# Optimization experiments

Measured on AMD Instinct MI355X. Metric: run time of the kernel, lower is better.

The kernel has to match this reference:

```python
import jax, jax.numpy as jnp
import numpy as np

H = 8        # num attention heads
DH = 160     # head dim (hidden_size // H)
HS = 1280    # hidden_size
CAD = 768    # cross_attention_dim
R = 4        # LoRA rank
LORA_SCALE = 1.0  # `scale` forward arg (default 1.0)


def setup_inputs() -> dict:
    key = jax.random.key(0)
    ks = jax.random.split(key, 16)
    rn = lambda k, s, std=0.02: (jax.random.normal(k, s) * std).astype(jnp.float32)
    return {
        "hidden_states": jax.random.normal(ks[0], (8, 4096, HS), jnp.float32),
        "encoder_hidden_states": jax.random.normal(ks[1], (8, 77, CAD), jnp.float32),
        # base attention projections (nn.Linear weight layout: [out, in])
        "Wq": rn(ks[2], (HS, HS)),
        "Wk": rn(ks[3], (HS, CAD)),
        "Wv": rn(ks[4], (HS, CAD)),
        "Wo": rn(ks[5], (HS, HS)),
        "bo": jnp.zeros((HS,), jnp.float32),
        # LoRA down/up pairs (down std ~ 1/rank; up nonzero so grads flow)
        "q_down": rn(ks[6], (R, HS), 0.25), "q_up": rn(ks[7], (HS, R)),
        "k_down": rn(ks[8], (R, CAD), 0.25), "k_up": rn(ks[9], (HS, R)),
        "v_down": rn(ks[10], (R, CAD), 0.25), "v_up": rn(ks[11], (HS, R)),
        "o_down": rn(ks[12], (R, HS), 0.25), "o_up": rn(ks[13], (HS, R)),
    }


def reference(hidden_states, encoder_hidden_states, Wq, Wk, Wv, Wo, bo,
              q_down, q_up, k_down, k_up, v_down, v_up, o_down, o_up):
    B, S, _ = hidden_states.shape
    T = encoder_hidden_states.shape[1]
    lora = lambda x, d, u: (x @ d.T) @ u.T  # LoRALinearLayer: up(down(x))

    q = hidden_states @ Wq.T + LORA_SCALE * lora(hidden_states, q_down, q_up)
    k = encoder_hidden_states @ Wk.T + LORA_SCALE * lora(encoder_hidden_states, k_down, k_up)
    v = encoder_hidden_states @ Wv.T + LORA_SCALE * lora(encoder_hidden_states, v_down, v_up)

    q = q.reshape(B, S, H, DH)
    k = k.reshape(B, T, H, DH)
    v = v.reshape(B, T, H, DH)

    # attn.get_attention_scores: scaled QK^T, softmax (no mask)
    inv_sqrt_d = jnp.asarray(1.0 / np.sqrt(DH), q.dtype)
    scores = jnp.einsum('bshd,bthd->bhst', q, k) * inv_sqrt_d
    probs = jax.nn.softmax(scores, axis=-1)
    o = jnp.einsum('bhst,bthd->bshd', probs, v).reshape(B, S, H * DH)

    # to_out[0] (Linear with bias) + LoRA on the same input; to_out[1] dropout = identity (eval)
    return o @ Wo.T + bo + LORA_SCALE * lora(o, o_down, o_up)
```

## Files before the change

kernel.cpp:

```cpp
#include <hip/hip_runtime.h>
#include <hip/hip_bf16.h>
#include <stdint.h>

typedef short bf16x8 __attribute__((ext_vector_type(8)));
typedef float f32x4 __attribute__((ext_vector_type(4)));

#define DEVI static __device__ __forceinline__

DEVI ushort f2bf(float f) {
  union { float f; uint32_t u; } v; v.f = f;
  uint32_t u = v.u;
  return (ushort)((u + 0x7fffu + ((u >> 16) & 1u)) >> 16);
}

DEVI void gload16(const void* g, void* l) {
  __builtin_amdgcn_global_load_lds((const __attribute__((address_space(1))) void*)g,
                                   (__attribute__((address_space(3))) void*)l,
                                   16, 0, 0);
}

#define SB() __builtin_amdgcn_sched_barrier(0)
#define BAR() __builtin_amdgcn_s_barrier()
#define MFMA(a, b, c) __builtin_amdgcn_mfma_f32_16x16x32_bf16((a), (b), (c), 0, 0, 0)

DEVI int pair_src_row(int c, int* k8) {
  int pair = c >> 3;
  int s = (c & 7) ^ (pair & 7);
  *k8 = s >> 1;
  return pair * 2 + (s & 1);
}
DEVI int pair_frag_off(int r, int k8) {
  int p = (k8 * 2 + (r & 1)) ^ ((r >> 1) & 7);
  return (r >> 1) * 64 + p * 8;
}

__global__ __launch_bounds__(256) void prep(
    const float* __restrict__ hs, ushort* __restrict__ hs_bf,
    const float* __restrict__ Wq, const float* __restrict__ q_up, const float* __restrict__ q_down,
    ushort* __restrict__ WqT, float scale,
    const float* __restrict__ ehs, ushort* __restrict__ ehs_bf,
    const float* __restrict__ Wk, const float* __restrict__ k_up, const float* __restrict__ k_down,
    const float* __restrict__ Wv, const float* __restrict__ v_up, const float* __restrict__ v_down,
    ushort* __restrict__ Wkv,
    const float* __restrict__ Wo, const float* __restrict__ o_up, const float* __restrict__ o_down,
    ushort* __restrict__ Wo_bf, ushort* __restrict__ Nt)
{
  __shared__ ushort tile[64][66];
  const int b = blockIdx.x;
  const int tid = threadIdx.x;
  if (b < 2048) {
    const long step = 2048L * 256;
    for (long idx = (long)b * 256 + tid; idx < 5242880; idx += step) {
      const float4* p = (const float4*)(hs + idx * 8);
      float4 a = p[0], c = p[1];
      union { ushort us[8]; uint4 v; } r;
      r.us[0] = f2bf(a.x); r.us[1] = f2bf(a.y); r.us[2] = f2bf(a.z); r.us[3] = f2bf(a.w);
      r.us[4] = f2bf(c.x); r.us[5] = f2bf(c.y); r.us[6] = f2bf(c.z); r.us[7] = f2bf(c.w);
      *(uint4*)(hs_bf + idx * 8) = r.v;
    }
  } else if (b < 2448) {
    const int fb = b - 2048;
    const int o0 = (fb / 20) * 64, i0 = (fb % 20) * 64;
    const int lo = tid >> 6;
    const int li = tid & 63;
#pragma unroll
    for (int r = 0; r < 16; ++r) {
      int o = o0 + r * 4 + lo;
      int i = i0 + li;
      float v = Wq[(long)o * 1280 + i];
#pragma unroll
      for (int q = 0; q < 4; ++q) v += q_up[o * 4 + q] * q_down[q * 1280 + i];
      tile[li][r * 4 + lo] = f2bf(v * scale);
    }
    __syncthreads();
#pragma unroll
    for (int r = 0; r < 16; ++r) {
      int i = i0 + r * 4 + lo;
      WqT[(long)i * 1280 + o0 + li] = tile[r * 4 + lo][li];
    }
  } else {
    const int sb = b - 2448;
    if (sb < 231) {
      int idx = sb * 256 + tid;
      if (idx < 59136) {
        const float4* p = (const float4*)(ehs + (long)idx * 8);
        float4 a = p[0], c = p[1];
        union { ushort us[8]; uint4 v; } r;
        r.us[0] = f2bf(a.x); r.us[1] = f2bf(a.y); r.us[2] = f2bf(a.z); r.us[3] = f2bf(a.w);
        r.us[4] = f2bf(c.x); r.us[5] = f2bf(c.y); r.us[6] = f2bf(c.z); r.us[7] = f2bf(c.w);
        *(uint4*)(ehs_bf + (long)idx * 8) = r.v;
      }
    } else if (sb < 4071) {
      int idx = (sb - 231) * 256 + tid;
      int o = idx / 768, i = idx - o * 768;
      float v = Wk[idx];
#pragma unroll
      for (int q = 0; q < 4; ++q) v += k_up[o * 4 + q] * k_down[q * 768 + i];
      Wkv[idx] = f2bf(v);
    } else if (sb < 7911) {
      int idx = (sb - 4071) * 256 + tid;
      int o = idx / 768, i = idx - o * 768;
      float v = Wv[idx];
#pragma unroll
      for (int q = 0; q < 4; ++q) v += v_up[o * 4 + q] * v_down[q * 768 + i];
      Wkv[983040 + idx] = f2bf(v);
    } else if (sb < 14311) {
      int idx = (sb - 7911) * 256 + tid;
      int o = idx / 1280, i = idx - o * 1280;
      float v = Wo[idx];
#pragma unroll
      for (int q = 0; q < 4; ++q) v += o_up[o * 4 + q] * o_down[q * 1280 + i];
      Wo_bf[idx] = f2bf(v);
    } else {
      int idx = (sb - 14311) * 256 + tid;
      int bb = idx / (1280 * 24);
      int rem = idx % (1280 * 24);
      int j = rem / 24, q = rem % 24;
      int h = q / 3, t = 77 + q % 3;
      Nt[(long)bb * 1280 * 640 + (long)j * 640 + h * 80 + t] = 0;
    }
  }
}


DEVI void gemm_bt_body(int bx, int by, int z,
    const ushort* __restrict__ A, long sA0, long sA1, int lda, int validM,
    const ushort* __restrict__ B, long sB0, long sB1, int ldb, int validN,
    float* __restrict__ C32, ushort* __restrict__ C16, long sC0, long sC1, int ldc,
    const float* __restrict__ bias, int K, ushort* As, ushort* Bs)
{
  const ushort* Ab = A + (long)(z >> 3) * sA0 + (long)(z & 7) * sA1;
  const ushort* Bb = B + (long)(z >> 3) * sB0 + (long)(z & 7) * sB1;
  const int m0 = bx * 128;
  const int n0 = by * 128;
  const int tid = threadIdx.x;
  const int lane = tid & 63;
  const int wid = tid >> 6;

  const int c0 = tid;
  const int arow0 = min(m0 + (c0 >> 2), validM - 1);
  const int arow1 = min(m0 + (c0 >> 2) + 64, validM - 1);
  const int brow0 = min(n0 + (c0 >> 2), validN - 1);
  const int brow1 = min(n0 + (c0 >> 2) + 64, validN - 1);
  const int seg = (c0 & 3) * 8;

  const int wr = (wid >> 1) * 64;
  const int wc = (wid & 1) * 64;
  const int frow = lane & 15;
  const int fk = (lane >> 4) * 8;

  f32x4 acc[4][4] = {};

  for (int kt = 0; kt < K; kt += 32) {
    gload16(Ab + (long)arow0 * lda + kt + seg, As + c0 * 8);
    gload16(Ab + (long)arow1 * lda + kt + seg, As + (c0 + 256) * 8);
    gload16(Bb + (long)brow0 * ldb + kt + seg, Bs + c0 * 8);
    gload16(Bb + (long)brow1 * ldb + kt + seg, Bs + (c0 + 256) * 8);
    __syncthreads();

    bf16x8 af[4], bfr[4];
#pragma unroll
    for (int m = 0; m < 4; ++m)
      af[m] = *(const bf16x8*)(As + (wr + m * 16 + frow) * 32 + fk);
#pragma unroll
    for (int n = 0; n < 4; ++n)
      bfr[n] = *(const bf16x8*)(Bs + (wc + n * 16 + frow) * 32 + fk);
#pragma unroll
    for (int m = 0; m < 4; ++m)
#pragma unroll
      for (int n = 0; n < 4; ++n)
        acc[m][n] = MFMA(af[m], bfr[n], acc[m][n]);
    __syncthreads();
  }

  const long cb = (long)(z >> 3) * sC0 + (long)(z & 7) * sC1;
  const int crow = m0 + wr + (lane >> 4) * 4;
  const int ccol = n0 + wc + (lane & 15);
#pragma unroll
  for (int m = 0; m < 4; ++m)
#pragma unroll
    for (int n = 0; n < 4; ++n)
#pragma unroll
      for (int j = 0; j < 4; ++j) {
        int r = crow + m * 16 + j;
        int c = ccol + n * 16;
        if (r < validM && c < validN) {
          float v = acc[m][n][j];
          if (bias) v += bias[c];
          if (C32) C32[cb + (long)r * ldc + c] = v;
          else     C16[cb + (long)r * ldc + c] = f2bf(v);
        }
      }
}

__global__ __launch_bounds__(256) void gemm_bt(
    const ushort* A, long sA0, long sA1, int lda, int validM,
    const ushort* B, long sB0, long sB1, int ldb, int validN,
    float* C32, ushort* C16, long sC0, long sC1, int ldc,
    const float* bias, int K)
{
  __shared__ ushort As[128 * 32];
  __shared__ ushort Bs[128 * 32];
  gemm_bt_body(blockIdx.x, blockIdx.y, blockIdx.z,
               A, sA0, sA1, lda, validM, B, sB0, sB1, ldb, validN,
               C32, C16, sC0, sC1, ldc, bias, K, As, Bs);
}

__global__ __launch_bounds__(256) void gemm_mtnt(
    const ushort* __restrict__ kv_bf, const ushort* __restrict__ WqT,
    const ushort* __restrict__ Wo_bf, ushort* __restrict__ Mt, ushort* __restrict__ Nt)
{
  __shared__ ushort As[128 * 32];
  __shared__ ushort Bs[128 * 32];
  const int x = blockIdx.x, z = blockIdx.z;
  if (x < 10) {
    gemm_bt_body(x, 0, z, Wo_bf, 0, 160, 1280, 1280,
                 kv_bf + 1280, 77L * 2560, 160, 2560, 77,
                 nullptr, Nt, 1280L * 640, 80, 640, nullptr, 160, As, Bs);
  } else {
    gemm_bt_body(0, x - 10, z, kv_bf, 77L * 2560, 160, 2560, 77,
                 WqT, 0, 160, 1280, 1280,
                 nullptr, Mt, 640L * 1280, 77L * 1280, 1280, nullptr, 160, As, Bs);
  }
}

__global__ __launch_bounds__(256, 3) void score_softmax(
    const ushort* __restrict__ hsb, const ushort* __restrict__ Mt,
    ushort* __restrict__ probs)
{
  __shared__ ushort lds[22528];

  const int z = blockIdx.z;
  const int s0 = blockIdx.x * 128;
  const int h0 = blockIdx.y * 2;
  const int tid = threadIdx.x;
  const int lane = tid & 63;
  const int wid = tid >> 6;
  const int wM = wid >> 1;
  const int wN = wid & 1;
  const int l15 = lane & 15;
  const int l4 = lane >> 4;

  const ushort* Ag = hsb + ((long)z * 4096 + s0) * 1280;
  long asrc[2]; int adst[2];
#pragma unroll
  for (int j = 0; j < 2; ++j) {
    int c = j * 256 + tid, k8;
    int r = pair_src_row(c, &k8);
    asrc[j] = (long)r * 1280 + k8 * 8;
    adst[j] = c * 8;
  }
  const ushort* Bg = Mt + (long)z * (640L * 1280);
  long bsrc[3]; int bdst[3];
#pragma unroll
  for (int j = 0; j < 3; ++j) {
    int c = j * 256 + tid, k8;
    int rb = pair_src_row(c, &k8);
    int hh = h0 + (rb >= 96);
    int tt = min(rb - 96 * (rb >= 96), 76);
    bsrc[j] = (long)(hh * 77 + tt) * 1280 + k8 * 8;
    bdst[j] = 4096 + c * 8;
  }

  int aoff[4], boff[6];
#pragma unroll
  for (int m = 0; m < 4; ++m)
    aoff[m] = pair_frag_off(wM * 64 + m * 16 + l15, l4);
#pragma unroll
  for (int n = 0; n < 6; ++n)
    boff[n] = 4096 + pair_frag_off(wN * 96 + n * 16 + l15, l4);

  f32x4 acc[4][6] = {};

#define SS_STAGE(bb, kt) { \
    _Pragma("unroll") for (int j = 0; j < 2; ++j) gload16(Ag + asrc[j] + (kt), &lds[(bb) + adst[j]]); \
    _Pragma("unroll") for (int j = 0; j < 3; ++j) gload16(Bg + bsrc[j] + (kt), &lds[(bb) + bdst[j]]); }

  SS_STAGE(0, 0)

  for (int t = 0; t < 40; ++t) {
    const int base = (t & 1) * 10240;
    if (t + 1 < 40) {
      SS_STAGE(10240 - base, (t + 1) * 32)
      asm volatile("s_waitcnt vmcnt(5)" ::: "memory");
    } else {
      asm volatile("s_waitcnt vmcnt(0)" ::: "memory");
    }
    SB(); BAR(); SB();
    bf16x8 av[4], bv[6];
#pragma unroll
    for (int m = 0; m < 4; ++m) av[m] = *(const bf16x8*)(&lds[base + aoff[m]]);
#pragma unroll
    for (int n = 0; n < 6; ++n) bv[n] = *(const bf16x8*)(&lds[base + boff[n]]);
    __builtin_amdgcn_s_setprio(1);
#pragma unroll
    for (int m = 0; m < 4; ++m)
#pragma unroll
      for (int n = 0; n < 6; ++n)
        acc[m][n] = MFMA(av[m], bv[n], acc[m][n]);
    __builtin_amdgcn_s_setprio(0);
    SB(); BAR();
  }
#undef SS_STAGE

#pragma unroll
  for (int m = 0; m < 4; ++m)
#pragma unroll
    for (int j = 0; j < 4; ++j) {
      float mx = -1e30f;
#pragma unroll
      for (int n = 0; n < 6; ++n)
        if (n * 16 + l15 < 77) mx = fmaxf(mx, acc[m][n][j]);
#pragma unroll
      for (int o = 8; o; o >>= 1) mx = fmaxf(mx, __shfl_xor(mx, o));
      float sum = 0.f;
#pragma unroll
      for (int n = 0; n < 6; ++n) {
        float e = (n * 16 + l15 < 77) ? __expf(acc[m][n][j] - mx) : 0.f;
        acc[m][n][j] = e;
        sum += e;
      }
#pragma unroll
      for (int o = 8; o; o >>= 1) sum += __shfl_xor(sum, o);
      float inv = 1.f / sum;
#pragma unroll
      for (int n = 0; n < 6; ++n) acc[m][n][j] *= inv;
    }

  __syncthreads();
  ushort* pw = lds + wid * 5632;
#pragma unroll
  for (int m = 0; m < 4; ++m)
#pragma unroll
    for (int n = 0; n < 5; ++n)
#pragma unroll
      for (int j = 0; j < 4; ++j)
        pw[(m * 16 + l4 * 4 + j) * 88 + n * 16 + l15] = f2bf(acc[m][n][j]);

  const uint* pw32 = (const uint*)pw;
  uint* probs32 = (uint*)probs;
  const int head = h0 + wN;
  const long sbase = (long)z * 4096 + s0 + wM * 64;
#pragma unroll 4
  for (int k = 0; k < 40; ++k) {
    int f2 = k * 64 + lane;
    int r = f2 / 40;
    int tp = f2 - r * 40;
    probs32[(sbase + r) * 320 + head * 40 + tp] = pw32[r * 44 + tp];
  }
}

__global__ __launch_bounds__(256, 4) void gemm_out(
    const ushort* __restrict__ P, const ushort* __restrict__ Nt,
    float* __restrict__ C, const float* __restrict__ bias)
{
  __shared__ ushort lds[17408];

  const int z = blockIdx.z;
  const ushort* Ab = P + (long)z * (4096L * 640) + (long)blockIdx.x * 128 * 640;
  const ushort* Bb = Nt + (long)z * (1280L * 640) + (long)blockIdx.y * 128 * 640;
  const int tid = threadIdx.x;
  const int lane = tid & 63;
  const int wid = tid >> 6;
  const int wM = wid >> 1;
  const int wN = wid & 1;
  const int l15 = lane & 15;
  const int l4 = lane >> 4;

  long asrc[2]; int adst[2], bdst[2];
#pragma unroll
  for (int j = 0; j < 2; ++j) {
    int c = j * 256 + tid, k8;
    int r = pair_src_row(c, &k8);
    asrc[j] = (long)r * 640 + k8 * 8;
    adst[j] = c * 8;
    bdst[j] = 4096 + c * 8;
  }

  int aoff[4], boff[4];
#pragma unroll
  for (int m = 0; m < 4; ++m)
    aoff[m] = pair_frag_off(wM * 64 + m * 16 + l15, l4);
#pragma unroll
  for (int n = 0; n < 4; ++n)
    boff[n] = 4096 + pair_frag_off(wN * 64 + n * 16 + l15, l4);

  f32x4 acc[4][4] = {};

#define OG_STAGE(bb, kt) { \
    _Pragma("unroll") for (int j = 0; j < 2; ++j) gload16(Ab + asrc[j] + (kt), &lds[(bb) + adst[j]]); \
    _Pragma("unroll") for (int j = 0; j < 2; ++j) gload16(Bb + asrc[j] + (kt), &lds[(bb) + bdst[j]]); }

  OG_STAGE(0, 0)

  for (int t = 0; t < 20; ++t) {
    const int base = (t & 1) * 8192;
    if (t + 1 < 20) {
      OG_STAGE(8192 - base, (t + 1) * 32)
      asm volatile("s_waitcnt vmcnt(4)" ::: "memory");
    } else {
      asm volatile("s_waitcnt vmcnt(0)" ::: "memory");
    }
    SB(); BAR(); SB();
    bf16x8 av[4], bv[4];
#pragma unroll
    for (int m = 0; m < 4; ++m) av[m] = *(const bf16x8*)(&lds[base + aoff[m]]);
#pragma unroll
    for (int n = 0; n < 4; ++n) bv[n] = *(const bf16x8*)(&lds[base + boff[n]]);
    __builtin_amdgcn_s_setprio(1);
#pragma unroll
    for (int m = 0; m < 4; ++m)
#pragma unroll
      for (int n = 0; n < 4; ++n)
        acc[m][n] = MFMA(av[m], bv[n], acc[m][n]);
    __builtin_amdgcn_s_setprio(0);
    SB(); BAR();
  }
#undef OG_STAGE

  __syncthreads();
  float* pw = (float*)lds + wid * 1088;
  const int ccol = blockIdx.y * 128 + wN * 64;
  const float4 bv4 = *(const float4*)(bias + ccol + l15 * 4);
  const long crow0 = (long)z * 4096 + blockIdx.x * 128 + wM * 64;
#pragma unroll
  for (int m = 0; m < 4; ++m) {
#pragma unroll
    for (int n = 0; n < 4; ++n)
#pragma unroll
      for (int j = 0; j < 4; ++j)
        pw[(l4 * 4 + j) * 68 + n * 16 + l15] = acc[m][n][j];
    asm volatile("s_waitcnt lgkmcnt(0)" ::: "memory"); SB();
#pragma unroll
    for (int pass = 0; pass < 4; ++pass) {
      int r = pass * 4 + l4;
      float4 v = *(const float4*)(pw + r * 68 + l15 * 4);
      v.x += bv4.x; v.y += bv4.y; v.z += bv4.z; v.w += bv4.w;
      *(float4*)(C + (crow0 + m * 16 + r) * 1280 + ccol + l15 * 4) = v;
    }
    asm volatile("s_waitcnt lgkmcnt(0)" ::: "memory"); SB();
  }
}

extern "C" void kernel_launch(void* const* d_in, const int* in_sizes, int n_in,
                              void* d_out, int out_size, void* d_ws, size_t ws_size,
                              hipStream_t stream) {
  (void)in_sizes; (void)n_in; (void)out_size; (void)ws_size;
  const float* hs     = (const float*)d_in[0];
  const float* ehs    = (const float*)d_in[1];
  const float* Wq     = (const float*)d_in[2];
  const float* Wk     = (const float*)d_in[3];
  const float* Wv     = (const float*)d_in[4];
  const float* Wo     = (const float*)d_in[5];
  const float* bo     = (const float*)d_in[6];
  const float* q_down = (const float*)d_in[7];
  const float* q_up   = (const float*)d_in[8];
  const float* k_down = (const float*)d_in[9];
  const float* k_up   = (const float*)d_in[10];
  const float* v_down = (const float*)d_in[11];
  const float* v_up   = (const float*)d_in[12];
  const float* o_down = (const float*)d_in[13];
  const float* o_up   = (const float*)d_in[14];

  char* w = (char*)d_ws;
  size_t off = 0;
  auto alloc = [&](size_t b) { char* p = w + off; off = (off + b + 255) & ~(size_t)255; return p; };
  ushort* hs_bf  = (ushort*)alloc(32768L * 1280 * 2);
  ushort* ehs_bf = (ushort*)alloc(616L * 768 * 2);
  ushort* WqT    = (ushort*)alloc(1280L * 1280 * 2);
  ushort* Wkv    = (ushort*)alloc(2560L * 768 * 2);
  ushort* Wo_bf  = (ushort*)alloc(1280L * 1280 * 2);
  ushort* kv_bf  = (ushort*)alloc(616L * 2560 * 2);
  ushort* Mt     = (ushort*)alloc(8L * 640 * 1280 * 2);
  ushort* Nt     = (ushort*)alloc(8L * 1280 * 640 * 2);
  ushort* probs  = (ushort*)alloc(8L * 4096 * 640 * 2);
  float*  outp   = (float*)d_out;
  const float invs = 0.07905694150420949f;

  prep<<<17719, 256, 0, stream>>>(hs, hs_bf, Wq, q_up, q_down, WqT, invs,
      ehs, ehs_bf, Wk, k_up, k_down, Wv, v_up, v_down, Wkv,
      Wo, o_up, o_down, Wo_bf, Nt);
  gemm_bt<<<dim3(5, 20, 1), 256, 0, stream>>>(ehs_bf, 0, 0, 768, 616,
      Wkv, 0, 0, 768, 2560, nullptr, kv_bf, 0, 0, 2560, nullptr, 768);
  gemm_mtnt<<<dim3(20, 1, 64), 256, 0, stream>>>(kv_bf, WqT, Wo_bf, Mt, Nt);
  score_softmax<<<dim3(32, 4, 8), 256, 0, stream>>>(hs_bf, Mt, probs);
  gemm_out<<<dim3(32, 10, 8), 256, 0, stream>>>(probs, Nt, outp, bo);
}
```

Baseline: 297.3 us.

## Fuse hidden_states bf16 conversion into score_softmax A-tile loading

Drops the separate pass that converts hidden_states to a bf16 buffer. score_softmax now loads fp32 hidden_states into registers, converts them to bf16 and writes them to LDS while the MFMAs of the previous stage run. The weight-folding prep work is split into a transpose-fold kernel for Wq and a kernel for the smaller conversions. This removes a 168MB fp32 read plus an 84MB bf16 write and read round trip. In exchange each score block now reads twice the A bytes, and the conversion ALU work runs inside the GEMM loop.

```diff
diff --git a/kernel.cpp b/kernel.cpp
--- a/kernel.cpp
+++ b/kernel.cpp
@@ -34,10 +34,32 @@
   return (r >> 1) * 64 + p * 8;
 }
 
-__global__ __launch_bounds__(256) void prep(
-    const float* __restrict__ hs, ushort* __restrict__ hs_bf,
-    const float* __restrict__ Wq, const float* __restrict__ q_up, const float* __restrict__ q_down,
-    ushort* __restrict__ WqT, float scale,
+__global__ __launch_bounds__(256) void fold_t(
+    const float* __restrict__ W, const float* __restrict__ up,
+    const float* __restrict__ down, ushort* __restrict__ outT, float scale)
+{
+  __shared__ ushort tile[64][66];
+  const int o0 = blockIdx.x * 64, i0 = blockIdx.y * 64;
+  const int lo = threadIdx.x >> 6;
+  const int li = threadIdx.x & 63;
+#pragma unroll
+  for (int r = 0; r < 16; ++r) {
+    int o = o0 + r * 4 + lo;
+    int i = i0 + li;
+    float v = W[(long)o * 1280 + i];
+#pragma unroll
+    for (int q = 0; q < 4; ++q) v += up[o * 4 + q] * down[q * 1280 + i];
+    tile[li][r * 4 + lo] = f2bf(v * scale);
+  }
+  __syncthreads();
+#pragma unroll
+  for (int r = 0; r < 16; ++r) {
+    int i = i0 + r * 4 + lo;
+    outT[(long)i * 1280 + o0 + li] = tile[r * 4 + lo][li];
+  }
+}
+
+__global__ __launch_bounds__(256) void smalls(
     const float* __restrict__ ehs, ushort* __restrict__ ehs_bf,
     const float* __restrict__ Wk, const float* __restrict__ k_up, const float* __restrict__ k_down,
     const float* __restrict__ Wv, const float* __restrict__ v_up, const float* __restrict__ v_down,
@@ -45,80 +67,46 @@
     const float* __restrict__ Wo, const float* __restrict__ o_up, const float* __restrict__ o_down,
     ushort* __restrict__ Wo_bf, ushort* __restrict__ Nt)
 {
-  __shared__ ushort tile[64][66];
   const int b = blockIdx.x;
   const int tid = threadIdx.x;
-  if (b < 2048) {
-    const long step = 2048L * 256;
-    for (long idx = (long)b * 256 + tid; idx < 5242880; idx += step) {
-      const float4* p = (const float4*)(hs + idx * 8);
+  if (b < 231) {
+    int idx = b * 256 + tid;
+    if (idx < 59136) {
+      const float4* p = (const float4*)(ehs + (long)idx * 8);
       float4 a = p[0], c = p[1];
       union { ushort us[8]; uint4 v; } r;
       r.us[0] = f2bf(a.x); r.us[1] = f2bf(a.y); r.us[2] = f2bf(a.z); r.us[3] = f2bf(a.w);
       r.us[4] = f2bf(c.x); r.us[5] = f2bf(c.y); r.us[6] = f2bf(c.z); r.us[7] = f2bf(c.w);
-      *(uint4*)(hs_bf + idx * 8) = r.v;
+      *(uint4*)(ehs_bf + (long)idx * 8) = r.v;
     }
-  } else if (b < 2448) {
-    const int fb = b - 2048;
-    const int o0 = (fb / 20) * 64, i0 = (fb % 20) * 64;
-    const int lo = tid >> 6;
-    const int li = tid & 63;
-#pragma unroll
-    for (int r = 0; r < 16; ++r) {
-      int o = o0 + r * 4 + lo;
-      int i = i0 + li;
-      float v = Wq[(long)o * 1280 + i];
-#pragma unroll
-      for (int q = 0; q < 4; ++q) v += q_up[o * 4 + q] * q_down[q * 1280 + i];
-      tile[li][r * 4 + lo] = f2bf(v * scale);
-    }
-    __syncthreads();
-#pragma unroll
-    for (int r = 0; r < 16; ++r) {
-      int i = i0 + r * 4 + lo;
-      WqT[(long)i * 1280 + o0 + li] = tile[r * 4 + lo][li];
-    }
+  } else if (b < 4071) {
+    int idx = (b - 231) * 256 + tid;
+    int o = idx / 768, i = idx - o * 768;
+    float v = Wk[idx];
+#pragma unroll
+    for (int q = 0; q < 4; ++q) v += k_up[o * 4 + q] * k_down[q * 768 + i];
+    Wkv[idx] = f2bf(v);
+  } else if (b < 7911) {
+    int idx = (b - 4071) * 256 + tid;
+    int o = idx / 768, i = idx - o * 768;
+    float v = Wv[idx];
+#pragma unroll
+    for (int q = 0; q < 4; ++q) v += v_up[o * 4 + q] * v_down[q * 768 + i];
+    Wkv[983040 + idx] = f2bf(v);
+  } else if (b < 14311) {
+    int idx = (b - 7911) * 256 + tid;
+    int o = idx / 1280, i = idx - o * 1280;
+    float v = Wo[idx];
+#pragma unroll
+    for (int q = 0; q < 4; ++q) v += o_up[o * 4 + q] * o_down[q * 1280 + i];
+    Wo_bf[idx] = f2bf(v);
   } else {
-    const int sb = b - 2448;
-    if (sb < 231) {
-      int idx = sb * 256 + tid;
-      if (idx < 59136) {
-        const float4* p = (const float4*)(ehs + (long)idx * 8);
-        float4 a = p[0], c = p[1];
-        union { ushort us[8]; uint4 v; } r;
-        r.us[0] = f2bf(a.x); r.us[1] = f2bf(a.y); r.us[2] = f2bf(a.z); r.us[3] = f2bf(a.w);
-        r.us[4] = f2bf(c.x); r.us[5] = f2bf(c.y); r.us[6] = f2bf(c.z); r.us[7] = f2bf(c.w);
-        *(uint4*)(ehs_bf + (long)idx * 8) = r.v;
-      }
-    } else if (sb < 4071) {
-      int idx = (sb - 231) * 256 + tid;
-      int o = idx / 768, i = idx - o * 768;
-      float v = Wk[idx];
-#pragma unroll
-      for (int q = 0; q < 4; ++q) v += k_up[o * 4 + q] * k_down[q * 768 + i];
-      Wkv[idx] = f2bf(v);
-    } else if (sb < 7911) {
-      int idx = (sb - 4071) * 256 + tid;
-      int o = idx / 768, i = idx - o * 768;
-      float v = Wv[idx];
-#pragma unroll
-      for (int q = 0; q < 4; ++q) v += v_up[o * 4 + q] * v_down[q * 768 + i];
-      Wkv[983040 + idx] = f2bf(v);
-    } else if (sb < 14311) {
-      int idx = (sb - 7911) * 256 + tid;
-      int o = idx / 1280, i = idx - o * 1280;
-      float v = Wo[idx];
-#pragma unroll
-      for (int q = 0; q < 4; ++q) v += o_up[o * 4 + q] * o_down[q * 1280 + i];
-      Wo_bf[idx] = f2bf(v);
-    } else {
-      int idx = (sb - 14311) * 256 + tid;
-      int bb = idx / (1280 * 24);
-      int rem = idx % (1280 * 24);
-      int j = rem / 24, q = rem % 24;
-      int h = q / 3, t = 77 + q % 3;
-      Nt[(long)bb * 1280 * 640 + (long)j * 640 + h * 80 + t] = 0;
-    }
+    int idx = (b - 14311) * 256 + tid;
+    int bb = idx / (1280 * 24);
+    int rem = idx % (1280 * 24);
+    int j = rem / 24, q = rem % 24;
+    int h = q / 3, t = 77 + q % 3;
+    Nt[(long)bb * 1280 * 640 + (long)j * 640 + h * 80 + t] = 0;
   }
 }
 
@@ -225,7 +213,7 @@
 }
 
 __global__ __launch_bounds__(256, 3) void score_softmax(
-    const ushort* __restrict__ hsb, const ushort* __restrict__ Mt,
+    const float* __restrict__ hsf, const ushort* __restrict__ Mt,
     ushort* __restrict__ probs)
 {
   __shared__ ushort lds[22528];
@@ -241,15 +229,11 @@
   const int l15 = lane & 15;
   const int l4 = lane >> 4;
 
-  const ushort* Ag = hsb + ((long)z * 4096 + s0) * 1280;
-  long asrc[2]; int adst[2];
-#pragma unroll
-  for (int j = 0; j < 2; ++j) {
-    int c = j * 256 + tid, k8;
-    int r = pair_src_row(c, &k8);
-    asrc[j] = (long)r * 1280 + k8 * 8;
-    adst[j] = c * 8;
-  }
+  const int ar = tid >> 1, ah = tid & 1;
+  const float* Ag = hsf + ((long)z * 4096 + s0 + ar) * 1280 + 16 * ah;
+  const int awoff0 = pair_frag_off(ar, 2 * ah);
+  const int awoff1 = pair_frag_off(ar, 2 * ah + 1);
+
   const ushort* Bg = Mt + (long)z * (640L * 1280);
   long bsrc[3]; int bdst[3];
 #pragma unroll
@@ -271,18 +255,38 @@
     boff[n] = 4096 + pair_frag_off(wN * 96 + n * 16 + l15, l4);
 
   f32x4 acc[4][6] = {};
-
-#define SS_STAGE(bb, kt) { \
-    _Pragma("unroll") for (int j = 0; j < 2; ++j) gload16(Ag + asrc[j] + (kt), &lds[(bb) + adst[j]]); \
-    _Pragma("unroll") for (int j = 0; j < 3; ++j) gload16(Bg + bsrc[j] + (kt), &lds[(bb) + bdst[j]]); }
-
-  SS_STAGE(0, 0)
+  float4 pa0, pa1, pa2, pa3;
+
+#define SS_LOADA(kt) { const float* p_ = Ag + (kt); \
+    pa0 = *(const float4*)(p_);     pa1 = *(const float4*)(p_ + 4); \
+    pa2 = *(const float4*)(p_ + 8); pa3 = *(const float4*)(p_ + 12); }
+#define SS_GLB(bb, kt) { _Pragma("unroll") for (int j = 0; j < 3; ++j) \
+    gload16(Bg + bsrc[j] + (kt), &lds[(bb) + bdst[j]]); }
+#define SS_CVTW(bb) { \
+    union { ushort us[8]; bf16x8 v; } c0_, c1_; \
+    c0_.us[0]=f2bf(pa0.x); c0_.us[1]=f2bf(pa0.y); c0_.us[2]=f2bf(pa0.z); c0_.us[3]=f2bf(pa0.w); \
+    c0_.us[4]=f2bf(pa1.x); c0_.us[5]=f2bf(pa1.y); c0_.us[6]=f2bf(pa1.z); c0_.us[7]=f2bf(pa1.w); \
+    c1_.us[0]=f2bf(pa2.x); c1_.us[1]=f2bf(pa2.y); c1_.us[2]=f2bf(pa2.z); c1_.us[3]=f2bf(pa2.w); \
+    c1_.us[4]=f2bf(pa3.x); c1_.us[5]=f2bf(pa3.y); c1_.us[6]=f2bf(pa3.z); c1_.us[7]=f2bf(pa3.w); \
+    *(bf16x8*)(&lds[(bb) + awoff0]) = c0_.v; \
+    *(bf16x8*)(&lds[(bb) + awoff1]) = c1_.v; }
+
+  SS_LOADA(0)
+  SB();
+  SS_GLB(0, 0)
+  SB();
+  SS_CVTW(0)
+  asm volatile("s_waitcnt lgkmcnt(0)" ::: "memory");
 
   for (int t = 0; t < 40; ++t) {
     const int base = (t & 1) * 10240;
+    const int nb = 10240 - base;
     if (t + 1 < 40) {
-      SS_STAGE(10240 - base, (t + 1) * 32)
-      asm volatile("s_waitcnt vmcnt(5)" ::: "memory");
+      const int kt1 = (t + 1) * 32;
+      SS_LOADA(kt1)
+      SB();
+      SS_GLB(nb, kt1)
+      asm volatile("s_waitcnt vmcnt(7)" ::: "memory");
     } else {
       asm volatile("s_waitcnt vmcnt(0)" ::: "memory");
     }
@@ -299,9 +303,14 @@
       for (int n = 0; n < 6; ++n)
         acc[m][n] = MFMA(av[m], bv[n], acc[m][n]);
     __builtin_amdgcn_s_setprio(0);
+    SB();
+    if (t + 1 < 40) { SS_CVTW(nb) }
+    asm volatile("s_waitcnt lgkmcnt(0)" ::: "memory");
     SB(); BAR();
   }
-#undef SS_STAGE
+#undef SS_LOADA
+#undef SS_GLB
+#undef SS_CVTW
 
 #pragma unroll
   for (int m = 0; m < 4; ++m)
@@ -465,7 +474,6 @@
   char* w = (char*)d_ws;
   size_t off = 0;
   auto alloc = [&](size_t b) { char* p = w + off; off = (off + b + 255) & ~(size_t)255; return p; };
-  ushort* hs_bf  = (ushort*)alloc(32768L * 1280 * 2);
   ushort* ehs_bf = (ushort*)alloc(616L * 768 * 2);
   ushort* WqT    = (ushort*)alloc(1280L * 1280 * 2);
   ushort* Wkv    = (ushort*)alloc(2560L * 768 * 2);
@@ -477,12 +485,13 @@
   float*  outp   = (float*)d_out;
   const float invs = 0.07905694150420949f;
 
-  prep<<<17719, 256, 0, stream>>>(hs, hs_bf, Wq, q_up, q_down, WqT, invs,
-      ehs, ehs_bf, Wk, k_up, k_down, Wv, v_up, v_down, Wkv,
+  fold_t<<<dim3(20, 20), 256, 0, stream>>>(Wq, q_up, q_down, WqT, invs);
+  smalls<<<15271, 256, 0, stream>>>(ehs, ehs_bf,
+      Wk, k_up, k_down, Wv, v_up, v_down, Wkv,
       Wo, o_up, o_down, Wo_bf, Nt);
   gemm_bt<<<dim3(5, 20, 1), 256, 0, stream>>>(ehs_bf, 0, 0, 768, 616,
       Wkv, 0, 0, 768, 2560, nullptr, kv_bf, 0, 0, 2560, nullptr, 768);
   gemm_mtnt<<<dim3(20, 1, 64), 256, 0, stream>>>(kv_bf, WqT, Wo_bf, Mt, Nt);
-  score_softmax<<<dim3(32, 4, 8), 256, 0, stream>>>(hs_bf, Mt, probs);
+  score_softmax<<<dim3(32, 4, 8), 256, 0, stream>>>(hs, Mt, probs);
   gemm_out<<<dim3(32, 10, 8), 256, 0, stream>>>(probs, Nt, outp, bo);
 }
```

New measurement: 285.2 us. -4.1%, faster.
